# Kernel optimization log

Measured on AMD Instinct MI355X. Metric: run time of the kernel, lower is better.

The kernel has to match this reference:

```python
import jax, jax.numpy as jnp
import numpy as np

N = 49998      # num nodes, divisible by (neg_sample_ratio + 2) = 3
E = 800000     # num edges (avg degree 16)
DIM_IN = 128
DIM_OUT = 32
H0 = 8         # heads layer 0
H1 = 1         # heads layer 1


def setup_inputs() -> dict:
    key = jax.random.key(0)
    ks = jax.random.split(key, 16)
    s = 0.05
    x = jax.random.normal(ks[0], (N, DIM_IN), dtype=jnp.float32)
    src = jax.random.randint(ks[1], (E,), 0, N)
    dst = jax.random.randint(ks[2], (E,), 0, N)
    W0 = jax.random.normal(ks[3], (DIM_IN, H0 * DIM_OUT), dtype=jnp.float32) * s
    al0 = jax.random.normal(ks[4], (H0, DIM_OUT), dtype=jnp.float32) * s
    ar0 = jax.random.normal(ks[5], (H0, DIM_OUT), dtype=jnp.float32) * s
    b0 = jnp.zeros((H0 * DIM_OUT,), dtype=jnp.float32)
    W1 = jax.random.normal(ks[6], (H0 * DIM_OUT, H1 * DIM_OUT), dtype=jnp.float32) * s
    al1 = jax.random.normal(ks[7], (H1, DIM_OUT), dtype=jnp.float32) * s
    ar1 = jax.random.normal(ks[8], (H1, DIM_OUT), dtype=jnp.float32) * s
    b1 = jnp.zeros((H1 * DIM_OUT,), dtype=jnp.float32)
    P1 = jax.random.normal(ks[9], (DIM_OUT, DIM_OUT), dtype=jnp.float32) * s
    pb1 = jnp.zeros((DIM_OUT,), dtype=jnp.float32)
    P2 = jax.random.normal(ks[10], (DIM_OUT, DIM_OUT), dtype=jnp.float32) * s
    pb2 = jnp.zeros((DIM_OUT,), dtype=jnp.float32)
    P3 = jax.random.normal(ks[11], (DIM_OUT, 1), dtype=jnp.float32) * s
    pb3 = jnp.zeros((1,), dtype=jnp.float32)
    return dict(x=x, src=src, dst=dst, neg_sample_ratio=1,
                W0=W0, al0=al0, ar0=ar0, b0=b0,
                W1=W1, al1=al1, ar1=ar1, b1=b1,
                P1=P1, pb1=pb1, P2=P2, pb2=pb2, P3=P3, pb3=pb3)


def gat_conv(x, src, dst, W, al, ar, b):
    """DGL GATConv: linear proj -> edge LeakyReLU score -> per-dst segment softmax -> weighted scatter-sum + bias."""
    n = x.shape[0]
    H, D = al.shape
    f = (x @ W).reshape(n, H, D)                     # [N,H,D]
    el = jnp.sum(f * al, axis=-1)                    # [N,H]
    er = jnp.sum(f * ar, axis=-1)                    # [N,H]
    e = jax.nn.leaky_relu(el[src] + er[dst], 0.2)    # [E,H] edge scores
    m = jax.ops.segment_max(e, dst, num_segments=n)  # [N,H] stable softmax max
    a = jnp.exp(e - m[dst])                          # [E,H]
    denom = jax.ops.segment_sum(a, dst, num_segments=n)  # [N,H]
    a = a / denom[dst]                               # normalized attention
    out = jax.ops.segment_sum(a[:, :, None] * f[src], dst, num_segments=n)  # [N,H,D]
    return out + b.reshape(1, H, D)


def reference(x, src, dst, neg_sample_ratio,
              W0, al0, ar0, b0, W1, al1, ar1, b1,
              P1, pb1, P2, pb2, P3, pb3):
    # layer 0: GATConv with ELU activation, flatten heads
    h = jax.nn.elu(gat_conv(x, src, dst, W0, al0, ar0, b0)).reshape(x.shape[0], -1)
    # layer 1: GATConv, no activation, mean over heads
    h = gat_conv(h, src, dst, W1, al1, ar1, b1).mean(axis=1)  # [N, DIM_OUT]

    num_edge = h.shape[0] // (neg_sample_ratio + 2)
    src_h = h[:num_edge]
    pos_dst_h = h[num_edge:2 * num_edge]
    neg_dst_h = h[2 * num_edge:]

    def predictor(z):
        z = jax.nn.relu(z @ P1 + pb1)
        z = jax.nn.relu(z @ P2 + pb2)
        return z @ P3 + pb3

    h_pos = predictor(src_h * pos_dst_h)
    h_neg = predictor(jnp.tile(src_h, (neg_sample_ratio, 1)) * neg_dst_h)
    return (h_pos, h_neg)
```

## Files before the change

### kernel.cpp

```cpp
#include <hip/hip_runtime.h>
#include <hip/hip_fp16.h>
#include <cmath>

#define CAPB 64
#define CAPF 88
#define CAP1 96
#define WA   92
#define G0_ROWS 32
#define G0_PAD 36
#define NSCAT 1024

typedef _Float16 h2v __attribute__((ext_vector_type(2)));

__device__ __forceinline__ float dot2a(unsigned f, unsigned w, float acc) {
  return __builtin_amdgcn_fdot2(__builtin_bit_cast(h2v, f),
                                __builtin_bit_cast(h2v, w), acc, false);
}
__device__ __forceinline__ unsigned pkh2(float lo, float hi) {
  return (unsigned)__half_as_ushort(__float2half_rn(lo)) |
         ((unsigned)__half_as_ushort(__float2half_rn(hi)) << 16);
}

__global__ void k_prep(const float* __restrict__ W0, const float* __restrict__ W1,
                       unsigned* __restrict__ W0h, unsigned* __restrict__ W1ct,
                       int* __restrict__ cnt, int Np1) {
  int gid = blockIdx.x * 256 + threadIdx.x;
  int stride = gridDim.x * 256;
  for (int i = gid; i < Np1; i += stride) cnt[i] = 0;
  if (gid < 16384) {
    int k2 = gid >> 8, c = gid & 255;
    W0h[gid] = pkh2(W0[(size_t)(2 * k2) * 256 + c], W0[(size_t)(2 * k2 + 1) * 256 + c]);
  } else if (gid < 20480) {
    int j = gid - 16384;
    int c = j >> 7, k2 = j & 127;
    W1ct[j] = pkh2(W1[(size_t)(2 * k2) * 32 + c], W1[(size_t)(2 * k2 + 1) * 32 + c]);
  } else if (gid < 20992) {
    W0h[gid - 20992 + 16896] = 0;
  }
}

__global__ void k_gemm0_scatter(const float* __restrict__ x, const unsigned* __restrict__ W0h,
                                const float* __restrict__ al, const float* __restrict__ ar,
                                const int* __restrict__ dst, const int* __restrict__ src,
                                unsigned short* __restrict__ f0h, float* __restrict__ el,
                                float* __restrict__ er, int* __restrict__ cnt,
                                int* __restrict__ ovf_cnt, int* __restrict__ bpad,
                                int* __restrict__ ovf, int N, int E, int ngemm) {
  __shared__ unsigned s_x2[66 * G0_PAD];
  int t = threadIdx.x;

  if (blockIdx.x >= ngemm) {
    int nscat = gridDim.x - ngemm;
    for (int e = (blockIdx.x - ngemm) * blockDim.x + t; e < E; e += nscat * blockDim.x) {
      int d = dst[e];
      int pos = atomicAdd(&cnt[d], 1);
      if (pos < CAPB) bpad[(size_t)d * CAPB + pos] = src[e];
      else { int op = atomicAdd(ovf_cnt, 1); ovf[op] = e; }
    }
    return;
  }

  int w = t >> 6, l = t & 63;
  int row0 = blockIdx.x * G0_ROWS;
  {
    int row = t & 31, cg = t >> 5;
    int grow = row0 + row; if (grow >= N) grow = N - 1;
    const float* xp = x + (size_t)grow * 128 + cg * 16;
    int k2b = cg * 8;
#pragma unroll
    for (int j = 0; j < 4; ++j) {
      float4 v = *(const float4*)(xp + 4 * j);
      s_x2[(k2b + 2 * j) * G0_PAD + row] = pkh2(v.x, v.y);
      s_x2[(k2b + 2 * j + 1) * G0_PAD + row] = pkh2(v.z, v.w);
    }
  }
  __syncthreads();

  float4 acc[8];
#pragma unroll
  for (int r = 0; r < 8; ++r) acc[r] = make_float4(0.f, 0.f, 0.f, 0.f);

  const unsigned* wp = W0h + 4 * l;
  int rbase = w * 8;

#define LDX(dstv, kk)                                              \
  { const unsigned* xk_ = &s_x2[(kk) * G0_PAD + rbase];            \
    *(uint4*)&dstv[0]  = *(const uint4*)(xk_);                     \
    *(uint4*)&dstv[4]  = *(const uint4*)(xk_ + 4); }
#define DOTS(xv, w4)                                               \
  _Pragma("unroll")                                                \
  for (int r = 0; r < 8; ++r) {                                    \
    acc[r].x = dot2a(xv[r], w4.x, acc[r].x);                       \
    acc[r].y = dot2a(xv[r], w4.y, acc[r].y);                       \
    acc[r].z = dot2a(xv[r], w4.z, acc[r].z);                       \
    acc[r].w = dot2a(xv[r], w4.w, acc[r].w);                       \
  }

  unsigned xA[8], xB[8];
  uint4 wA = *(const uint4*)(wp);
  uint4 wB = *(const uint4*)(wp + 256);
  LDX(xA, 0);
#pragma unroll 2
  for (int k2 = 0; k2 < 64; k2 += 2) {
    uint4 wC = *(const uint4*)(wp + (size_t)(k2 + 2) * 256);
    uint4 wD = *(const uint4*)(wp + (size_t)(k2 + 3) * 256);
    LDX(xB, k2 + 1);
    DOTS(xA, wA);
    LDX(xA, k2 + 2);
    DOTS(xB, wB);
    wA = wC; wB = wD;
  }
#undef LDX
#undef DOTS

  int hh = l >> 3;
  float4 al4 = *(const float4*)(al + 4 * l);
  float4 ar4 = *(const float4*)(ar + 4 * l);
#pragma unroll
  for (int r = 0; r < 8; ++r) {
    int row = row0 + rbase + r;
    float4 f = acc[r];
    if (row < N) {
      ushort4 h4;
      h4.x = __half_as_ushort(__float2half_rn(f.x));
      h4.y = __half_as_ushort(__float2half_rn(f.y));
      h4.z = __half_as_ushort(__float2half_rn(f.z));
      h4.w = __half_as_ushort(__float2half_rn(f.w));
      *(ushort4*)(f0h + (size_t)row * 256 + 4 * l) = h4;
    }
    float pl = fmaf(f.x, al4.x, fmaf(f.y, al4.y, fmaf(f.z, al4.z, f.w * al4.w)));
    float pr = fmaf(f.x, ar4.x, fmaf(f.y, ar4.y, fmaf(f.z, ar4.z, f.w * ar4.w)));
#pragma unroll
    for (int off = 4; off >= 1; off >>= 1) {
      pl += __shfl_xor(pl, off, 64);
      pr += __shfl_xor(pr, off, 64);
    }
    if ((l & 7) == 0 && row < N) {
      el[row * 8 + hh] = pl;
      er[row * 8 + hh] = pr;
    }
  }
}

__global__ void k_fused0(const float* __restrict__ el, const float* __restrict__ er,
                         const unsigned short* __restrict__ f0h, const int* __restrict__ cnt,
                         const int* __restrict__ ovf_cnt, const int* __restrict__ bpad,
                         const int* __restrict__ ovf, const int* __restrict__ dstp,
                         const int* __restrict__ src, const float* __restrict__ b0,
                         const unsigned* __restrict__ W1ct, const float* __restrict__ al1,
                         const float* __restrict__ ar1, unsigned short* __restrict__ f1h,
                         float* __restrict__ el1, float* __restrict__ er1, int N) {
  __shared__ unsigned s_w1[32 * 132];
  __shared__ unsigned short s_wa[8][8 * WA];
  __shared__ int s_s[8][CAPF];
  __shared__ unsigned s_h2[8][128];

  const int t = threadIdx.x;
  for (int base = t * 4; base < 4096; base += 2048) {
    uint4 v = *(const uint4*)&W1ct[base];
    int c = base >> 7, k2 = base & 127;
    *(uint4*)&s_w1[c * 132 + k2] = v;
  }
  __syncthreads();

  const int w = __builtin_amdgcn_readfirstlane(t >> 6);
  const int l = t & 63;
  const int n = blockIdx.x * 8 + w;
  if (n >= N) return;

  int* sS = s_s[w];
  unsigned short* sWA = s_wa[w];

  const int sub = l & 31, half = l >> 5, hh = sub >> 2;
  float4 b0a = ((const float4*)(b0 + 8 * sub))[0];
  float4 b0b = ((const float4*)(b0 + 8 * sub))[1];
  float al1c = al1[sub], ar1c = ar1[sub];

  int cn = cnt[n];
  int degb = cn < CAPB ? cn : CAPB;
  if (l < degb) sS[l] = bpad[(size_t)n * CAPB + l];
  int deg = degb;
  int ovl = ovf_cnt[0];
  if (ovl) {
    int d = degb;
    if (l == 0) {
      for (int j = 0; j < ovl && d < 84; ++j) {
        int e = ovf[j];
        if (dstp[e] == n) sS[d++] = src[e];
      }
    }
    deg = __shfl(d, 0, 64);
  }

  int degp = (deg + 3) & ~3;
  if (l < degp - deg) sS[deg + l] = sS[0];

#define GLOAD(AA, BB, ii)                                              \
  { int2 s_ = *(const int2*)&sS[(ii) + 2 * half];                      \
    AA = ((const uint4*)(f0h + (size_t)s_.x * 256))[sub];              \
    BB = ((const uint4*)(f0h + (size_t)s_.y * 256))[sub]; }
#define GCOMP(AA, BB, ii)                                              \
  { unsigned wpk = *(const unsigned*)&sWA[hh * WA + (ii) + 2 * half];  \
    unsigned lo_, hi_;                                                 \
    lo_ = __builtin_amdgcn_perm(AA.x, BB.x, 0x01000504u);              \
    hi_ = __builtin_amdgcn_perm(AA.x, BB.x, 0x03020706u);              \
    a0 = dot2a(lo_, wpk, a0); a1 = dot2a(hi_, wpk, a1);                \
    lo_ = __builtin_amdgcn_perm(AA.y, BB.y, 0x01000504u);              \
    hi_ = __builtin_amdgcn_perm(AA.y, BB.y, 0x03020706u);              \
    a2 = dot2a(lo_, wpk, a2); a3 = dot2a(hi_, wpk, a3);                \
    lo_ = __builtin_amdgcn_perm(AA.z, BB.z, 0x01000504u);              \
    hi_ = __builtin_amdgcn_perm(AA.z, BB.z, 0x03020706u);              \
    a4 = dot2a(lo_, wpk, a4); a5 = dot2a(hi_, wpk, a5);                \
    lo_ = __builtin_amdgcn_perm(AA.w, BB.w, 0x01000504u);              \
    hi_ = __builtin_amdgcn_perm(AA.w, BB.w, 0x03020706u);              \
    a6 = dot2a(lo_, wpk, a6); a7 = dot2a(hi_, wpk, a7); }

  uint4 A, B, A2, B2;
  if (degp > 0) {
    GLOAD(A, B, 0);
    if (degp > 4) GLOAD(A2, B2, 4);
  }

  float er_h = er[n * 8 + (l & 7)];
  float psum = 0.f;
  for (int e = l >> 3; e < deg; e += 8) {
    int sidx = sS[e];
    float v = el[sidx * 8 + (l & 7)] + er_h;
    v = v >= 0.f ? v : 0.2f * v;
    float a = __expf(v);
    sWA[(l & 7) * WA + e] = __half_as_ushort(__float2half_rn(a));
    psum += a;
  }
  psum += __shfl_xor(psum, 8, 64);
  psum += __shfl_xor(psum, 16, 64);
  psum += __shfl_xor(psum, 32, 64);
  float rs = psum > 0.f ? __builtin_amdgcn_rcpf(psum) : 0.f;

  { int pe = deg + (l >> 3); if (pe < degp) sWA[(l & 7) * WA + pe] = 0; }

  float a0 = 0.f, a1 = 0.f, a2 = 0.f, a3 = 0.f, a4 = 0.f, a5 = 0.f, a6 = 0.f, a7 = 0.f;
  if (degp > 0) {
    for (int i = 0;;) {
      GCOMP(A, B, i);
      if (i + 8 < degp) GLOAD(A, B, i + 8);
      if (i + 4 >= degp) break;
      GCOMP(A2, B2, i + 4);
      if (i + 12 < degp) GLOAD(A2, B2, i + 12);
      if (i + 8 >= degp) break;
      i += 8;
    }
  }
#undef GLOAD
#undef GCOMP
  a0 += __shfl_xor(a0, 32, 64); a1 += __shfl_xor(a1, 32, 64);
  a2 += __shfl_xor(a2, 32, 64); a3 += __shfl_xor(a3, 32, 64);
  a4 += __shfl_xor(a4, 32, 64); a5 += __shfl_xor(a5, 32, 64);
  a6 += __shfl_xor(a6, 32, 64); a7 += __shfl_xor(a7, 32, 64);

  float sc = __shfl(rs, hh, 64);
  float o0 = fmaf(a0, sc, b0a.x), o1 = fmaf(a1, sc, b0a.y);
  float o2 = fmaf(a2, sc, b0a.z), o3 = fmaf(a3, sc, b0a.w);
  float o4 = fmaf(a4, sc, b0b.x), o5 = fmaf(a5, sc, b0b.y);
  float o6 = fmaf(a6, sc, b0b.z), o7 = fmaf(a7, sc, b0b.w);
  o0 = o0 > 0.f ? o0 : __expf(o0) - 1.f;  o1 = o1 > 0.f ? o1 : __expf(o1) - 1.f;
  o2 = o2 > 0.f ? o2 : __expf(o2) - 1.f;  o3 = o3 > 0.f ? o3 : __expf(o3) - 1.f;
  o4 = o4 > 0.f ? o4 : __expf(o4) - 1.f;  o5 = o5 > 0.f ? o5 : __expf(o5) - 1.f;
  o6 = o6 > 0.f ? o6 : __expf(o6) - 1.f;  o7 = o7 > 0.f ? o7 : __expf(o7) - 1.f;
  if (half == 0) {
    uint4 hp;
    hp.x = pkh2(o0, o1); hp.y = pkh2(o2, o3);
    hp.z = pkh2(o4, o5); hp.w = pkh2(o6, o7);
    *(uint4*)&s_h2[w][4 * sub] = hp;
  }
  asm volatile("s_waitcnt lgkmcnt(0)" ::: "memory");

  const unsigned* wrow = &s_w1[sub * 132 + half * 64];
  const unsigned* hrow = &s_h2[w][half * 64];
  float p = 0.f;
#pragma unroll
  for (int j = 0; j < 64; j += 4) {
    uint4 wv = *(const uint4*)&wrow[j];
    uint4 hv = *(const uint4*)&hrow[j];
    p = dot2a(hv.x, wv.x, p);
    p = dot2a(hv.y, wv.y, p);
    p = dot2a(hv.z, wv.z, p);
    p = dot2a(hv.w, wv.w, p);
  }
  p += __shfl_xor(p, 32, 64);
  float pn = __shfl_xor(p, 1, 64);
  float pl = p * al1c, pr = p * ar1c;
#pragma unroll
  for (int off = 16; off >= 1; off >>= 1) {
    pl += __shfl_xor(pl, off, 64);
    pr += __shfl_xor(pr, off, 64);
  }
  if (half == 0 && (sub & 1) == 0)
    *(unsigned*)(f1h + (size_t)n * 32 + sub) = pkh2(p, pn);
  if (l == 0) { el1[n] = pl; er1[n] = pr; }
}

__global__ void k_fused1(const float* __restrict__ el, const float* __restrict__ er,
                         const unsigned short* __restrict__ f1h, const int* __restrict__ cnt,
                         const int* __restrict__ ovf_cnt, const int* __restrict__ bpad,
                         const int* __restrict__ ovf, const int* __restrict__ dstp,
                         const int* __restrict__ src, const float* __restrict__ b1,
                         float* __restrict__ h1, int N) {
  __shared__ int s_s[8][CAP1];
  __shared__ unsigned s_wp[8][CAP1 / 2];

  const int t = threadIdx.x;
  const int g = __builtin_amdgcn_readfirstlane(t >> 6);
  const int lane = t & 63;
  int n = blockIdx.x * 8 + g;
  int nn = n < N ? n : N - 1;
  int* sS = s_s[g];
  unsigned* sWP = s_wp[g];

  int cn = cnt[nn];
  int degb = cn < CAPB ? cn : CAPB;
  if (lane < degb) sS[lane] = bpad[(size_t)nn * CAPB + lane];
  int deg = degb;
  int ovl = ovf_cnt[0];
  if (ovl) {
    int d = degb;
    if (lane == 0) {
      for (int j = 0; j < ovl && d < CAP1 - 16; ++j) {
        int e = ovf[j];
        if (dstp[e] == nn) sS[d++] = src[e];
      }
    }
    deg = __shfl(d, 0, 64);
  }
  int degp = (deg + 15) & ~15;
  if (deg + lane < degp) sS[deg + lane] = sS[0];

  const int es = lane >> 3, q = lane & 7;
  uint2 A, B;
  if (degp > 0) {
    A = *(const uint2*)(f1h + (size_t)sS[es] * 32 + 4 * q);
    B = *(const uint2*)(f1h + (size_t)sS[es + 8] * 32 + 4 * q);
  }

  float er_n = er[nn];
  float psum = 0.f;
  for (int i0 = 0; i0 < degp; i0 += 64) {
    int i = i0 + lane;
    float a = 0.f;
    if (i < deg) {
      float v = el[sS[i]] + er_n;
      v = v >= 0.f ? v : 0.2f * v;
      a = __expf(v);
      psum += a;
    }
    float an = __shfl_xor(a, 8, 64);
    if ((lane & 15) < 8 && i < degp)
      sWP[(i0 >> 1) + ((lane >> 4) << 3) + (lane & 7)] = pkh2(a, an);
  }
#pragma unroll
  for (int off = 32; off >= 1; off >>= 1) psum += __shfl_xor(psum, off, 64);
  float rs = psum > 0.f ? __builtin_amdgcn_rcpf(psum) : 0.f;

  float c0 = 0.f, c1 = 0.f, c2 = 0.f, c3 = 0.f;
  if (degp > 0) {
    for (int i0 = 0;;) {
      int in = i0 + 16;
      uint2 A2, B2;
      if (in < degp) {
        A2 = *(const uint2*)(f1h + (size_t)sS[in + es] * 32 + 4 * q);
        B2 = *(const uint2*)(f1h + (size_t)sS[in + es + 8] * 32 + 4 * q);
      }
      unsigned wp = sWP[(i0 >> 1) + es];
      unsigned lo = __builtin_amdgcn_perm(A.x, B.x, 0x01000504u);
      unsigned hi = __builtin_amdgcn_perm(A.x, B.x, 0x03020706u);
      c0 = dot2a(lo, wp, c0); c1 = dot2a(hi, wp, c1);
      lo = __builtin_amdgcn_perm(A.y, B.y, 0x01000504u);
      hi = __builtin_amdgcn_perm(A.y, B.y, 0x03020706u);
      c2 = dot2a(lo, wp, c2); c3 = dot2a(hi, wp, c3);
      if (in >= degp) break;
      i0 = in; A = A2; B = B2;
    }
  }
#pragma unroll
  for (int off = 8; off <= 32; off <<= 1) {
    c0 += __shfl_xor(c0, off, 64); c1 += __shfl_xor(c1, off, 64);
    c2 += __shfl_xor(c2, off, 64); c3 += __shfl_xor(c3, off, 64);
  }
  if (es == 0 && n < N) {
    float4 b = *(const float4*)(b1 + 4 * q);
    float4 o;
    o.x = fmaf(c0, rs, b.x); o.y = fmaf(c1, rs, b.y);
    o.z = fmaf(c2, rs, b.z); o.w = fmaf(c3, rs, b.w);
    ((float4*)(h1 + (size_t)n * 32))[q] = o;
  }
}

__global__ void k_pred(const float* __restrict__ h1, const float* __restrict__ P1,
                       const float* __restrict__ pb1, const float* __restrict__ P2,
                       const float* __restrict__ pb2, const float* __restrict__ P3,
                       const float* __restrict__ pb3, float* __restrict__ out,
                       int num_edge, int total) {
  int t = threadIdx.x;
  int lane = t & 31, grp = t >> 5;
  int k = blockIdx.x * 8 + grp;
  int kk = k < total ? k : 0;
  float z;
  if (kk < num_edge) {
    z = h1[(size_t)kk * 32 + lane] * h1[(size_t)(kk + num_edge) * 32 + lane];
  } else {
    int i = kk - num_edge;
    int im = i;
    while (im >= num_edge) im -= num_edge;
    z = h1[(size_t)im * 32 + lane] * h1[(size_t)(2 * num_edge + i) * 32 + lane];
  }
  double a1 = 0;
#pragma unroll
  for (int d = 0; d < 32; ++d)
    a1 += (double)__shfl(z, d, 32) * (double)P1[d * 32 + lane];
  float t1 = (float)(a1 + (double)pb1[lane]);
  t1 = t1 > 0.f ? t1 : 0.f;
  double a2 = 0;
#pragma unroll
  for (int d = 0; d < 32; ++d)
    a2 += (double)__shfl(t1, d, 32) * (double)P2[d * 32 + lane];
  float t2 = (float)(a2 + (double)pb2[lane]);
  t2 = t2 > 0.f ? t2 : 0.f;
  double a3 = (double)t2 * (double)P3[lane];
#pragma unroll
  for (int off = 16; off >= 1; off >>= 1) a3 += __shfl_xor(a3, off, 64);
  if (lane == 0 && k < total) out[k] = (float)(a3 + (double)pb3[0]);
}

extern "C" void kernel_launch(void* const* d_in, const int* in_sizes, int n_in,
                              void* d_out, int out_size, void* d_ws, size_t ws_size,
                              hipStream_t stream) {
  const float* x   = (const float*)d_in[0];
  const int*   src = (const int*)d_in[1];
  const int*   dst = (const int*)d_in[2];
  const float* W0  = (const float*)d_in[4];
  const float* al0 = (const float*)d_in[5];
  const float* ar0 = (const float*)d_in[6];
  const float* b0  = (const float*)d_in[7];
  const float* W1  = (const float*)d_in[8];
  const float* al1 = (const float*)d_in[9];
  const float* ar1 = (const float*)d_in[10];
  const float* b1  = (const float*)d_in[11];
  const float* P1  = (const float*)d_in[12];
  const float* pb1 = (const float*)d_in[13];
  const float* P2  = (const float*)d_in[14];
  const float* pb2 = (const float*)d_in[15];
  const float* P3  = (const float*)d_in[16];
  const float* pb3 = (const float*)d_in[17];

  int N = in_sizes[0] / 128;
  int E = in_sizes[1];
  int num_edge = N - out_size;

  size_t off = 0;
  auto alloc = [&](size_t bytes) -> void* {
    void* p = (char*)d_ws + off;
    off += (bytes + 255) & ~(size_t)255;
    return p;
  };
  unsigned short* f0h = (unsigned short*)alloc((size_t)N * 256 * 2);
  unsigned short* f1h = (unsigned short*)alloc((size_t)N * 32 * 2);
  float* h1   = (float*)alloc((size_t)N * 32 * 4);
  float* el   = (float*)alloc((size_t)N * 8 * 4);
  float* er   = (float*)alloc((size_t)N * 8 * 4);
  float* el1  = (float*)alloc((size_t)N * 4);
  float* er1  = (float*)alloc((size_t)N * 4);
  int*   cnt  = (int*)alloc((size_t)(N + 1) * 4);
  int*   bpad = (int*)alloc((size_t)N * CAPB * 4);
  int*   ovf  = (int*)alloc((size_t)E * 4);
  unsigned* W1ct = (unsigned*)alloc(4096 * 4);
  unsigned* W0h  = (unsigned*)alloc(16896 * 4);
  if (off > ws_size) return;
  int* ovf_cnt = cnt + N;

  int ngemm = (N + G0_ROWS - 1) / G0_ROWS;
  k_prep<<<128, 256, 0, stream>>>(W0, W1, W0h, W1ct, cnt, N + 1);
  k_gemm0_scatter<<<ngemm + NSCAT, 256, 0, stream>>>(x, W0h, al0, ar0, dst, src,
                                            f0h, el, er, cnt, ovf_cnt, bpad, ovf,
                                            N, E, ngemm);
  k_fused0<<<(N + 7) / 8, 512, 0, stream>>>(el, er, f0h, cnt, ovf_cnt, bpad, ovf, dst,
                                            src, b0, W1ct, al1, ar1, f1h, el1, er1, N);
  k_fused1<<<(N + 7) / 8, 512, 0, stream>>>(el1, er1, f1h, cnt, ovf_cnt, bpad, ovf, dst,
                                            src, b1, h1, N);
  k_pred<<<(out_size + 7) / 8, 256, 0, stream>>>(h1, P1, pb1, P2, pb2, P3, pb3,
                                                 (float*)d_out, num_edge, out_size);
}
```

Before: 262.6 us.

## Split layer-1 projection out of fused aggregation kernel and shrink GEMM0 tile

```diff
diff --git a/kernel.cpp b/kernel.cpp
--- a/kernel.cpp
+++ b/kernel.cpp
@@ -6,7 +6,7 @@
 #define CAPF 88
 #define CAP1 96
 #define WA   92
-#define G0_ROWS 32
+#define G0_ROWS 16
 #define G0_PAD 36
 #define NSCAT 1024
 
@@ -63,12 +63,12 @@
   int w = t >> 6, l = t & 63;
   int row0 = blockIdx.x * G0_ROWS;
   {
-    int row = t & 31, cg = t >> 5;
+    int row = t & 15, cg = t >> 4;
     int grow = row0 + row; if (grow >= N) grow = N - 1;
-    const float* xp = x + (size_t)grow * 128 + cg * 16;
-    int k2b = cg * 8;
-#pragma unroll
-    for (int j = 0; j < 4; ++j) {
+    const float* xp = x + (size_t)grow * 128 + cg * 8;
+    int k2b = cg * 4;
+#pragma unroll
+    for (int j = 0; j < 2; ++j) {
       float4 v = *(const float4*)(xp + 4 * j);
       s_x2[(k2b + 2 * j) * G0_PAD + row] = pkh2(v.x, v.y);
       s_x2[(k2b + 2 * j + 1) * G0_PAD + row] = pkh2(v.z, v.w);
@@ -76,27 +76,25 @@
   }
   __syncthreads();
 
-  float4 acc[8];
-#pragma unroll
-  for (int r = 0; r < 8; ++r) acc[r] = make_float4(0.f, 0.f, 0.f, 0.f);
+  float4 acc[4];
+#pragma unroll
+  for (int r = 0; r < 4; ++r) acc[r] = make_float4(0.f, 0.f, 0.f, 0.f);
 
   const unsigned* wp = W0h + 4 * l;
-  int rbase = w * 8;
+  int rbase = w * 4;
 
 #define LDX(dstv, kk)                                              \
-  { const unsigned* xk_ = &s_x2[(kk) * G0_PAD + rbase];            \
-    *(uint4*)&dstv[0]  = *(const uint4*)(xk_);                     \
-    *(uint4*)&dstv[4]  = *(const uint4*)(xk_ + 4); }
+  { *(uint4*)&dstv[0] = *(const uint4*)&s_x2[(kk) * G0_PAD + rbase]; }
 #define DOTS(xv, w4)                                               \
   _Pragma("unroll")                                                \
-  for (int r = 0; r < 8; ++r) {                                    \
+  for (int r = 0; r < 4; ++r) {                                    \
     acc[r].x = dot2a(xv[r], w4.x, acc[r].x);                       \
     acc[r].y = dot2a(xv[r], w4.y, acc[r].y);                       \
     acc[r].z = dot2a(xv[r], w4.z, acc[r].z);                       \
     acc[r].w = dot2a(xv[r], w4.w, acc[r].w);                       \
   }
 
-  unsigned xA[8], xB[8];
+  unsigned xA[4], xB[4];
   uint4 wA = *(const uint4*)(wp);
   uint4 wB = *(const uint4*)(wp + 256);
   LDX(xA, 0);
@@ -117,7 +115,7 @@
   float4 al4 = *(const float4*)(al + 4 * l);
   float4 ar4 = *(const float4*)(ar + 4 * l);
 #pragma unroll
-  for (int r = 0; r < 8; ++r) {
+  for (int r = 0; r < 4; ++r) {
     int row = row0 + rbase + r;
     float4 f = acc[r];
     if (row < N) {
@@ -147,25 +145,14 @@
                          const int* __restrict__ ovf_cnt, const int* __restrict__ bpad,
                          const int* __restrict__ ovf, const int* __restrict__ dstp,
                          const int* __restrict__ src, const float* __restrict__ b0,
-                         const unsigned* __restrict__ W1ct, const float* __restrict__ al1,
-                         const float* __restrict__ ar1, unsigned short* __restrict__ f1h,
-                         float* __restrict__ el1, float* __restrict__ er1, int N) {
-  __shared__ unsigned s_w1[32 * 132];
-  __shared__ unsigned short s_wa[8][8 * WA];
-  __shared__ int s_s[8][CAPF];
-  __shared__ unsigned s_h2[8][128];
+                         unsigned* __restrict__ h2g, int N) {
+  __shared__ unsigned short s_wa[4][8 * WA];
+  __shared__ int s_s[4][CAPF];
 
   const int t = threadIdx.x;
-  for (int base = t * 4; base < 4096; base += 2048) {
-    uint4 v = *(const uint4*)&W1ct[base];
-    int c = base >> 7, k2 = base & 127;
-    *(uint4*)&s_w1[c * 132 + k2] = v;
-  }
-  __syncthreads();
-
   const int w = __builtin_amdgcn_readfirstlane(t >> 6);
   const int l = t & 63;
-  const int n = blockIdx.x * 8 + w;
+  const int n = blockIdx.x * 4 + w;
   if (n >= N) return;
 
   int* sS = s_s[w];
@@ -174,7 +161,6 @@
   const int sub = l & 31, half = l >> 5, hh = sub >> 2;
   float4 b0a = ((const float4*)(b0 + 8 * sub))[0];
   float4 b0b = ((const float4*)(b0 + 8 * sub))[1];
-  float al1c = al1[sub], ar1c = ar1[sub];
 
   int cn = cnt[n];
   int degb = cn < CAPB ? cn : CAPB;
@@ -270,33 +256,57 @@
     uint4 hp;
     hp.x = pkh2(o0, o1); hp.y = pkh2(o2, o3);
     hp.z = pkh2(o4, o5); hp.w = pkh2(o6, o7);
-    *(uint4*)&s_h2[w][4 * sub] = hp;
-  }
-  asm volatile("s_waitcnt lgkmcnt(0)" ::: "memory");
-
-  const unsigned* wrow = &s_w1[sub * 132 + half * 64];
-  const unsigned* hrow = &s_h2[w][half * 64];
+    *(uint4*)(h2g + (size_t)n * 128 + 4 * sub) = hp;
+  }
+}
+
+__global__ void k_gemm1(const unsigned* __restrict__ h2g, const unsigned* __restrict__ W1ct,
+                        const float* __restrict__ al1, const float* __restrict__ ar1,
+                        unsigned short* __restrict__ f1h, float* __restrict__ el1,
+                        float* __restrict__ er1, int N) {
+  __shared__ unsigned s_w1[32 * 132];
+  __shared__ unsigned s_h[8 * 128];
+
+  const int t = threadIdx.x;
+  const int n0 = blockIdx.x * 8;
+  for (int base = t * 4; base < 4096; base += 1024) {
+    uint4 v = *(const uint4*)&W1ct[base];
+    int c = base >> 7, k2 = base & 127;
+    *(uint4*)&s_w1[c * 132 + k2] = v;
+  }
+  {
+    int r = t >> 5, wi = t & 31;
+    int row = n0 + r; if (row >= N) row = N - 1;
+    uint4 v = *(const uint4*)(h2g + (size_t)row * 128 + wi * 4);
+    *(uint4*)&s_h[r * 128 + wi * 4] = v;
+  }
+  __syncthreads();
+
+  const int r = t >> 5, c = t & 31;
+  const int n = n0 + r;
+  const unsigned* hrow = &s_h[r * 128];
+  const unsigned* wrow = &s_w1[c * 132];
   float p = 0.f;
-#pragma unroll
-  for (int j = 0; j < 64; j += 4) {
+#pragma unroll 8
+  for (int j = 0; j < 128; j += 4) {
+    uint4 hv = *(const uint4*)&hrow[j];
     uint4 wv = *(const uint4*)&wrow[j];
-    uint4 hv = *(const uint4*)&hrow[j];
     p = dot2a(hv.x, wv.x, p);
     p = dot2a(hv.y, wv.y, p);
     p = dot2a(hv.z, wv.z, p);
     p = dot2a(hv.w, wv.w, p);
   }
-  p += __shfl_xor(p, 32, 64);
-  float pn = __shfl_xor(p, 1, 64);
-  float pl = p * al1c, pr = p * ar1c;
+  float pl = p * al1[c], pr = p * ar1[c];
 #pragma unroll
   for (int off = 16; off >= 1; off >>= 1) {
-    pl += __shfl_xor(pl, off, 64);
-    pr += __shfl_xor(pr, off, 64);
-  }
-  if (half == 0 && (sub & 1) == 0)
-    *(unsigned*)(f1h + (size_t)n * 32 + sub) = pkh2(p, pn);
-  if (l == 0) { el1[n] = pl; er1[n] = pr; }
+    pl += __shfl_xor(pl, off, 32);
+    pr += __shfl_xor(pr, off, 32);
+  }
+  float pn = __shfl_xor(p, 1, 32);
+  if (n < N) {
+    if ((c & 1) == 0) *(unsigned*)(f1h + (size_t)n * 32 + c) = pkh2(p, pn);
+    if (c == 0) { el1[n] = pl; er1[n] = pr; }
+  }
 }
 
 __global__ void k_fused1(const float* __restrict__ el, const float* __restrict__ er,
@@ -462,6 +472,7 @@
     return p;
   };
   unsigned short* f0h = (unsigned short*)alloc((size_t)N * 256 * 2);
+  unsigned* h2g = (unsigned*)alloc((size_t)N * 128 * 4);
   unsigned short* f1h = (unsigned short*)alloc((size_t)N * 32 * 2);
   float* h1   = (float*)alloc((size_t)N * 32 * 4);
   float* el   = (float*)alloc((size_t)N * 8 * 4);
@@ -481,8 +492,9 @@
   k_gemm0_scatter<<<ngemm + NSCAT, 256, 0, stream>>>(x, W0h, al0, ar0, dst, src,
                                             f0h, el, er, cnt, ovf_cnt, bpad, ovf,
                                             N, E, ngemm);
-  k_fused0<<<(N + 7) / 8, 512, 0, stream>>>(el, er, f0h, cnt, ovf_cnt, bpad, ovf, dst,
-                                            src, b0, W1ct, al1, ar1, f1h, el1, er1, N);
+  k_fused0<<<(N + 3) / 4, 256, 0, stream>>>(el, er, f0h, cnt, ovf_cnt, bpad, ovf, dst,
+                                            src, b0, h2g, N);
+  k_gemm1<<<(N + 7) / 8, 256, 0, stream>>>(h2g, W1ct, al1, ar1, f1h, el1, er1, N);
   k_fused1<<<(N + 7) / 8, 512, 0, stream>>>(el1, er1, f1h, cnt, ovf_cnt, bpad, ovf, dst,
                                             src, b1, h1, N);
   k_pred<<<(out_size + 7) / 8, 256, 0, stream>>>(h1, P1, pb1, P2, pb2, P3, pb3,
```

After: 295.2 us. +12.4%, slower.

## Stage W0 chunks through double-buffered LDS in layer-0 GEMM

Applied to the files above, without the earlier changes.

```diff
diff --git a/kernel.cpp b/kernel.cpp
--- a/kernel.cpp
+++ b/kernel.cpp
@@ -34,8 +34,6 @@
     int j = gid - 16384;
     int c = j >> 7, k2 = j & 127;
     W1ct[j] = pkh2(W1[(size_t)(2 * k2) * 32 + c], W1[(size_t)(2 * k2 + 1) * 32 + c]);
-  } else if (gid < 20992) {
-    W0h[gid - 20992 + 16896] = 0;
   }
 }
 
@@ -46,7 +44,8 @@
                                 float* __restrict__ er, int* __restrict__ cnt,
                                 int* __restrict__ ovf_cnt, int* __restrict__ bpad,
                                 int* __restrict__ ovf, int N, int E, int ngemm) {
-  __shared__ unsigned s_x2[66 * G0_PAD];
+  __shared__ unsigned s_x2[64 * G0_PAD];
+  __shared__ unsigned s_w0[2][8 * 256];
   int t = threadIdx.x;
 
   if (blockIdx.x >= ngemm) {
@@ -74,44 +73,42 @@
       s_x2[(k2b + 2 * j + 1) * G0_PAD + row] = pkh2(v.z, v.w);
     }
   }
-  __syncthreads();
 
   float4 acc[8];
 #pragma unroll
   for (int r = 0; r < 8; ++r) acc[r] = make_float4(0.f, 0.f, 0.f, 0.f);
 
-  const unsigned* wp = W0h + 4 * l;
   int rbase = w * 8;
 
-#define LDX(dstv, kk)                                              \
-  { const unsigned* xk_ = &s_x2[(kk) * G0_PAD + rbase];            \
-    *(uint4*)&dstv[0]  = *(const uint4*)(xk_);                     \
-    *(uint4*)&dstv[4]  = *(const uint4*)(xk_ + 4); }
-#define DOTS(xv, w4)                                               \
-  _Pragma("unroll")                                                \
-  for (int r = 0; r < 8; ++r) {                                    \
-    acc[r].x = dot2a(xv[r], w4.x, acc[r].x);                       \
-    acc[r].y = dot2a(xv[r], w4.y, acc[r].y);                       \
-    acc[r].z = dot2a(xv[r], w4.z, acc[r].z);                       \
-    acc[r].w = dot2a(xv[r], w4.w, acc[r].w);                       \
-  }
-
-  unsigned xA[8], xB[8];
-  uint4 wA = *(const uint4*)(wp);
-  uint4 wB = *(const uint4*)(wp + 256);
-  LDX(xA, 0);
-#pragma unroll 2
-  for (int k2 = 0; k2 < 64; k2 += 2) {
-    uint4 wC = *(const uint4*)(wp + (size_t)(k2 + 2) * 256);
-    uint4 wD = *(const uint4*)(wp + (size_t)(k2 + 3) * 256);
-    LDX(xB, k2 + 1);
-    DOTS(xA, wA);
-    LDX(xA, k2 + 2);
-    DOTS(xB, wB);
-    wA = wC; wB = wD;
-  }
-#undef LDX
-#undef DOTS
+  uint4 rA = *(const uint4*)(W0h + t * 4);
+  uint4 rB = *(const uint4*)(W0h + 1024 + t * 4);
+
+  for (int c = 0; c < 8; ++c) {
+    *(uint4*)&s_w0[c & 1][t * 4] = rA;
+    *(uint4*)&s_w0[c & 1][1024 + t * 4] = rB;
+    if (c + 1 < 8) {
+      rA = *(const uint4*)(W0h + (c + 1) * 2048 + t * 4);
+      rB = *(const uint4*)(W0h + (c + 1) * 2048 + 1024 + t * 4);
+    }
+    __syncthreads();
+    const unsigned* wb = s_w0[c & 1];
+#pragma unroll
+    for (int k2r = 0; k2r < 8; ++k2r) {
+      int k2 = c * 8 + k2r;
+      uint4 w4 = *(const uint4*)&wb[k2r * 256 + 4 * l];
+      unsigned xv[8];
+      const unsigned* xk_ = &s_x2[k2 * G0_PAD + rbase];
+      *(uint4*)&xv[0] = *(const uint4*)(xk_);
+      *(uint4*)&xv[4] = *(const uint4*)(xk_ + 4);
+#pragma unroll
+      for (int r = 0; r < 8; ++r) {
+        acc[r].x = dot2a(xv[r], w4.x, acc[r].x);
+        acc[r].y = dot2a(xv[r], w4.y, acc[r].y);
+        acc[r].z = dot2a(xv[r], w4.z, acc[r].z);
+        acc[r].w = dot2a(xv[r], w4.w, acc[r].w);
+      }
+    }
+  }
 
   int hh = l >> 3;
   float4 al4 = *(const float4*)(al + 4 * l);
@@ -472,7 +469,7 @@
   int*   bpad = (int*)alloc((size_t)N * CAPB * 4);
   int*   ovf  = (int*)alloc((size_t)E * 4);
   unsigned* W1ct = (unsigned*)alloc(4096 * 4);
-  unsigned* W0h  = (unsigned*)alloc(16896 * 4);
+  unsigned* W0h  = (unsigned*)alloc(16384 * 4);
   if (off > ws_size) return;
   int* ovf_cnt = cnt + N;
 
```

New measurement: 289.9 us. 10.4% more time.

## Use persistent grid-stride waves in fused GAT kernels with prefetch of next node's adjacency

Applied to the files above, without the earlier changes.

```diff
diff --git a/kernel.cpp b/kernel.cpp
--- a/kernel.cpp
+++ b/kernel.cpp
@@ -9,6 +9,7 @@
 #define G0_ROWS 32
 #define G0_PAD 36
 #define NSCAT 1024
+#define PBLK 1024
 
 typedef _Float16 h2v __attribute__((ext_vector_type(2)));
 
@@ -165,8 +166,9 @@
 
   const int w = __builtin_amdgcn_readfirstlane(t >> 6);
   const int l = t & 63;
-  const int n = blockIdx.x * 8 + w;
-  if (n >= N) return;
+  const int stride = gridDim.x * 8;
+  int node = blockIdx.x * 8 + w;
+  if (node >= N) return;
 
   int* sS = s_s[w];
   unsigned short* sWA = s_wa[w];
@@ -175,25 +177,10 @@
   float4 b0a = ((const float4*)(b0 + 8 * sub))[0];
   float4 b0b = ((const float4*)(b0 + 8 * sub))[1];
   float al1c = al1[sub], ar1c = ar1[sub];
-
-  int cn = cnt[n];
-  int degb = cn < CAPB ? cn : CAPB;
-  if (l < degb) sS[l] = bpad[(size_t)n * CAPB + l];
-  int deg = degb;
-  int ovl = ovf_cnt[0];
-  if (ovl) {
-    int d = degb;
-    if (l == 0) {
-      for (int j = 0; j < ovl && d < 84; ++j) {
-        int e = ovf[j];
-        if (dstp[e] == n) sS[d++] = src[e];
-      }
-    }
-    deg = __shfl(d, 0, 64);
-  }
-
-  int degp = (deg + 3) & ~3;
-  if (l < degp - deg) sS[deg + l] = sS[0];
+  const int ovl = ovf_cnt[0];
+
+  int cur_cn = cnt[node];
+  int cur_bp = bpad[(size_t)node * CAPB + l];
 
 #define GLOAD(AA, BB, ii)                                              \
   { int2 s_ = *(const int2*)&sS[(ii) + 2 * half];                      \
@@ -215,88 +202,119 @@
     hi_ = __builtin_amdgcn_perm(AA.w, BB.w, 0x03020706u);              \
     a6 = dot2a(lo_, wpk, a6); a7 = dot2a(hi_, wpk, a7); }
 
-  uint4 A, B, A2, B2;
-  if (degp > 0) {
-    GLOAD(A, B, 0);
-    if (degp > 4) GLOAD(A2, B2, 4);
-  }
-
-  float er_h = er[n * 8 + (l & 7)];
-  float psum = 0.f;
-  for (int e = l >> 3; e < deg; e += 8) {
-    int sidx = sS[e];
-    float v = el[sidx * 8 + (l & 7)] + er_h;
-    v = v >= 0.f ? v : 0.2f * v;
-    float a = __expf(v);
-    sWA[(l & 7) * WA + e] = __half_as_ushort(__float2half_rn(a));
-    psum += a;
-  }
-  psum += __shfl_xor(psum, 8, 64);
-  psum += __shfl_xor(psum, 16, 64);
-  psum += __shfl_xor(psum, 32, 64);
-  float rs = psum > 0.f ? __builtin_amdgcn_rcpf(psum) : 0.f;
-
-  { int pe = deg + (l >> 3); if (pe < degp) sWA[(l & 7) * WA + pe] = 0; }
-
-  float a0 = 0.f, a1 = 0.f, a2 = 0.f, a3 = 0.f, a4 = 0.f, a5 = 0.f, a6 = 0.f, a7 = 0.f;
-  if (degp > 0) {
-    for (int i = 0;;) {
-      GCOMP(A, B, i);
-      if (i + 8 < degp) GLOAD(A, B, i + 8);
-      if (i + 4 >= degp) break;
-      GCOMP(A2, B2, i + 4);
-      if (i + 12 < degp) GLOAD(A2, B2, i + 12);
-      if (i + 8 >= degp) break;
-      i += 8;
-    }
+  while (true) {
+    const int n = node;
+    int cn = cur_cn;
+    int bpv = cur_bp;
+    const int nxt = node + stride;
+    if (nxt < N) {
+      cur_cn = cnt[nxt];
+      cur_bp = bpad[(size_t)nxt * CAPB + l];
+    }
+
+    int degb = cn < CAPB ? cn : CAPB;
+    if (l < degb) sS[l] = bpv;
+    int deg = degb;
+    if (ovl) {
+      int d = degb;
+      if (l == 0) {
+        for (int j = 0; j < ovl && d < 84; ++j) {
+          int e = ovf[j];
+          if (dstp[e] == n) sS[d++] = src[e];
+        }
+      }
+      deg = __shfl(d, 0, 64);
+    }
+
+    int degp = (deg + 3) & ~3;
+    if (l < degp - deg) sS[deg + l] = sS[0];
+
+    uint4 A, B, A2, B2;
+    if (degp > 0) {
+      GLOAD(A, B, 0);
+      if (degp > 4) GLOAD(A2, B2, 4);
+    }
+
+    float er_h = er[n * 8 + (l & 7)];
+    float psum = 0.f;
+    for (int e = l >> 3; e < deg; e += 8) {
+      int sidx = sS[e];
+      float v = el[sidx * 8 + (l & 7)] + er_h;
+      v = v >= 0.f ? v : 0.2f * v;
+      float a = __expf(v);
+      sWA[(l & 7) * WA + e] = __half_as_ushort(__float2half_rn(a));
+      psum += a;
+    }
+    psum += __shfl_xor(psum, 8, 64);
+    psum += __shfl_xor(psum, 16, 64);
+    psum += __shfl_xor(psum, 32, 64);
+    float rs = psum > 0.f ? __builtin_amdgcn_rcpf(psum) : 0.f;
+
+    { int pe = deg + (l >> 3); if (pe < degp) sWA[(l & 7) * WA + pe] = 0; }
+
+    float a0 = 0.f, a1 = 0.f, a2 = 0.f, a3 = 0.f, a4 = 0.f, a5 = 0.f, a6 = 0.f, a7 = 0.f;
+    if (degp > 0) {
+      for (int i = 0;;) {
+        GCOMP(A, B, i);
+        if (i + 8 < degp) GLOAD(A, B, i + 8);
+        if (i + 4 >= degp) break;
+        GCOMP(A2, B2, i + 4);
+        if (i + 12 < degp) GLOAD(A2, B2, i + 12);
+        if (i + 8 >= degp) break;
+        i += 8;
+      }
+    }
+    a0 += __shfl_xor(a0, 32, 64); a1 += __shfl_xor(a1, 32, 64);
+    a2 += __shfl_xor(a2, 32, 64); a3 += __shfl_xor(a3, 32, 64);
+    a4 += __shfl_xor(a4, 32, 64); a5 += __shfl_xor(a5, 32, 64);
+    a6 += __shfl_xor(a6, 32, 64); a7 += __shfl_xor(a7, 32, 64);
+
+    float sc = __shfl(rs, hh, 64);
+    float o0 = fmaf(a0, sc, b0a.x), o1 = fmaf(a1, sc, b0a.y);
+    float o2 = fmaf(a2, sc, b0a.z), o3 = fmaf(a3, sc, b0a.w);
+    float o4 = fmaf(a4, sc, b0b.x), o5 = fmaf(a5, sc, b0b.y);
+    float o6 = fmaf(a6, sc, b0b.z), o7 = fmaf(a7, sc, b0b.w);
+    o0 = o0 > 0.f ? o0 : __expf(o0) - 1.f;  o1 = o1 > 0.f ? o1 : __expf(o1) - 1.f;
+    o2 = o2 > 0.f ? o2 : __expf(o2) - 1.f;  o3 = o3 > 0.f ? o3 : __expf(o3) - 1.f;
+    o4 = o4 > 0.f ? o4 : __expf(o4) - 1.f;  o5 = o5 > 0.f ? o5 : __expf(o5) - 1.f;
+    o6 = o6 > 0.f ? o6 : __expf(o6) - 1.f;  o7 = o7 > 0.f ? o7 : __expf(o7) - 1.f;
+    if (half == 0) {
+      uint4 hp;
+      hp.x = pkh2(o0, o1); hp.y = pkh2(o2, o3);
+      hp.z = pkh2(o4, o5); hp.w = pkh2(o6, o7);
+      *(uint4*)&s_h2[w][4 * sub] = hp;
+    }
+    asm volatile("s_waitcnt lgkmcnt(0)" ::: "memory");
+
+    const unsigned* wrow = &s_w1[sub * 132 + half * 64];
+    const unsigned* hrow = &s_h2[w][half * 64];
+    float p = 0.f;
+#pragma unroll
+    for (int j = 0; j < 64; j += 4) {
+      uint4 wv = *(const uint4*)&wrow[j];
+      uint4 hv = *(const uint4*)&hrow[j];
+      p = dot2a(hv.x, wv.x, p);
+      p = dot2a(hv.y, wv.y, p);
+      p = dot2a(hv.z, wv.z, p);
+      p = dot2a(hv.w, wv.w, p);
+    }
+    p += __shfl_xor(p, 32, 64);
+    float pn = __shfl_xor(p, 1, 64);
+    float pl = p * al1c, pr = p * ar1c;
+#pragma unroll
+    for (int off = 16; off >= 1; off >>= 1) {
+      pl += __shfl_xor(pl, off, 64);
+      pr += __shfl_xor(pr, off, 64);
+    }
+    if (half == 0 && (sub & 1) == 0)
+      *(unsigned*)(f1h + (size_t)n * 32 + sub) = pkh2(p, pn);
+    if (l == 0) { el1[n] = pl; er1[n] = pr; }
+
+    if (nxt >= N) break;
+    node = nxt;
   }
 #undef GLOAD
 #undef GCOMP
-  a0 += __shfl_xor(a0, 32, 64); a1 += __shfl_xor(a1, 32, 64);
-  a2 += __shfl_xor(a2, 32, 64); a3 += __shfl_xor(a3, 32, 64);
-  a4 += __shfl_xor(a4, 32, 64); a5 += __shfl_xor(a5, 32, 64);
-  a6 += __shfl_xor(a6, 32, 64); a7 += __shfl_xor(a7, 32, 64);
-
-  float sc = __shfl(rs, hh, 64);
-  float o0 = fmaf(a0, sc, b0a.x), o1 = fmaf(a1, sc, b0a.y);
-  float o2 = fmaf(a2, sc, b0a.z), o3 = fmaf(a3, sc, b0a.w);
-  float o4 = fmaf(a4, sc, b0b.x), o5 = fmaf(a5, sc, b0b.y);
-  float o6 = fmaf(a6, sc, b0b.z), o7 = fmaf(a7, sc, b0b.w);
-  o0 = o0 > 0.f ? o0 : __expf(o0) - 1.f;  o1 = o1 > 0.f ? o1 : __expf(o1) - 1.f;
-  o2 = o2 > 0.f ? o2 : __expf(o2) - 1.f;  o3 = o3 > 0.f ? o3 : __expf(o3) - 1.f;
-  o4 = o4 > 0.f ? o4 : __expf(o4) - 1.f;  o5 = o5 > 0.f ? o5 : __expf(o5) - 1.f;
-  o6 = o6 > 0.f ? o6 : __expf(o6) - 1.f;  o7 = o7 > 0.f ? o7 : __expf(o7) - 1.f;
-  if (half == 0) {
-    uint4 hp;
-    hp.x = pkh2(o0, o1); hp.y = pkh2(o2, o3);
-    hp.z = pkh2(o4, o5); hp.w = pkh2(o6, o7);
-    *(uint4*)&s_h2[w][4 * sub] = hp;
-  }
-  asm volatile("s_waitcnt lgkmcnt(0)" ::: "memory");
-
-  const unsigned* wrow = &s_w1[sub * 132 + half * 64];
-  const unsigned* hrow = &s_h2[w][half * 64];
-  float p = 0.f;
-#pragma unroll
-  for (int j = 0; j < 64; j += 4) {
-    uint4 wv = *(const uint4*)&wrow[j];
-    uint4 hv = *(const uint4*)&hrow[j];
-    p = dot2a(hv.x, wv.x, p);
-    p = dot2a(hv.y, wv.y, p);
-    p = dot2a(hv.z, wv.z, p);
-    p = dot2a(hv.w, wv.w, p);
-  }
-  p += __shfl_xor(p, 32, 64);
-  float pn = __shfl_xor(p, 1, 64);
-  float pl = p * al1c, pr = p * ar1c;
-#pragma unroll
-  for (int off = 16; off >= 1; off >>= 1) {
-    pl += __shfl_xor(pl, off, 64);
-    pr += __shfl_xor(pr, off, 64);
-  }
-  if (half == 0 && (sub & 1) == 0)
-    *(unsigned*)(f1h + (size_t)n * 32 + sub) = pkh2(p, pn);
-  if (l == 0) { el1[n] = pl; er1[n] = pr; }
 }
 
 __global__ void k_fused1(const float* __restrict__ el, const float* __restrict__ er,
@@ -311,86 +329,104 @@
   const int t = threadIdx.x;
   const int g = __builtin_amdgcn_readfirstlane(t >> 6);
   const int lane = t & 63;
-  int n = blockIdx.x * 8 + g;
-  int nn = n < N ? n : N - 1;
+  const int stride = gridDim.x * 8;
+  int node = blockIdx.x * 8 + g;
+  if (node >= N) return;
   int* sS = s_s[g];
   unsigned* sWP = s_wp[g];
 
-  int cn = cnt[nn];
-  int degb = cn < CAPB ? cn : CAPB;
-  if (lane < degb) sS[lane] = bpad[(size_t)nn * CAPB + lane];
-  int deg = degb;
-  int ovl = ovf_cnt[0];
-  if (ovl) {
-    int d = degb;
-    if (lane == 0) {
-      for (int j = 0; j < ovl && d < CAP1 - 16; ++j) {
-        int e = ovf[j];
-        if (dstp[e] == nn) sS[d++] = src[e];
+  const int es = lane >> 3, q = lane & 7;
+  const int ovl = ovf_cnt[0];
+  float4 bb = *(const float4*)(b1 + 4 * q);
+
+  int cur_cn = cnt[node];
+  int cur_bp = bpad[(size_t)node * CAPB + lane];
+
+  while (true) {
+    const int n = node;
+    int cn = cur_cn;
+    int bpv = cur_bp;
+    const int nxt = node + stride;
+    if (nxt < N) {
+      cur_cn = cnt[nxt];
+      cur_bp = bpad[(size_t)nxt * CAPB + lane];
+    }
+
+    int degb = cn < CAPB ? cn : CAPB;
+    if (lane < degb) sS[lane] = bpv;
+    int deg = degb;
+    if (ovl) {
+      int d = degb;
+      if (lane == 0) {
+        for (int j = 0; j < ovl && d < CAP1 - 16; ++j) {
+          int e = ovf[j];
+          if (dstp[e] == n) sS[d++] = src[e];
+        }
       }
-    }
-    deg = __shfl(d, 0, 64);
-  }
-  int degp = (deg + 15) & ~15;
-  if (deg + lane < degp) sS[deg + lane] = sS[0];
-
-  const int es = lane >> 3, q = lane & 7;
-  uint2 A, B;
-  if (degp > 0) {
-    A = *(const uint2*)(f1h + (size_t)sS[es] * 32 + 4 * q);
-    B = *(const uint2*)(f1h + (size_t)sS[es + 8] * 32 + 4 * q);
-  }
-
-  float er_n = er[nn];
-  float psum = 0.f;
-  for (int i0 = 0; i0 < degp; i0 += 64) {
-    int i = i0 + lane;
-    float a = 0.f;
-    if (i < deg) {
-      float v = el[sS[i]] + er_n;
-      v = v >= 0.f ? v : 0.2f * v;
-      a = __expf(v);
-      psum += a;
-    }
-    float an = __shfl_xor(a, 8, 64);
-    if ((lane & 15) < 8 && i < degp)
-      sWP[(i0 >> 1) + ((lane >> 4) << 3) + (lane & 7)] = pkh2(a, an);
-  }
-#pragma unroll
-  for (int off = 32; off >= 1; off >>= 1) psum += __shfl_xor(psum, off, 64);
-  float rs = psum > 0.f ? __builtin_amdgcn_rcpf(psum) : 0.f;
-
-  float c0 = 0.f, c1 = 0.f, c2 = 0.f, c3 = 0.f;
-  if (degp > 0) {
-    for (int i0 = 0;;) {
-      int in = i0 + 16;
-      uint2 A2, B2;
-      if (in < degp) {
-        A2 = *(const uint2*)(f1h + (size_t)sS[in + es] * 32 + 4 * q);
-        B2 = *(const uint2*)(f1h + (size_t)sS[in + es + 8] * 32 + 4 * q);
+      deg = __shfl(d, 0, 64);
+    }
+    int degp = (deg + 15) & ~15;
+    if (deg + lane < degp) sS[deg + lane] = sS[0];
+
+    uint2 A, B;
+    if (degp > 0) {
+      A = *(const uint2*)(f1h + (size_t)sS[es] * 32 + 4 * q);
+      B = *(const uint2*)(f1h + (size_t)sS[es + 8] * 32 + 4 * q);
+    }
+
+    float er_n = er[n];
+    float psum = 0.f;
+    for (int i0 = 0; i0 < degp; i0 += 64) {
+      int i = i0 + lane;
+      float a = 0.f;
+      if (i < deg) {
+        float v = el[sS[i]] + er_n;
+        v = v >= 0.f ? v : 0.2f * v;
+        a = __expf(v);
+        psum += a;
       }
-      unsigned wp = sWP[(i0 >> 1) + es];
-      unsigned lo = __builtin_amdgcn_perm(A.x, B.x, 0x01000504u);
-      unsigned hi = __builtin_amdgcn_perm(A.x, B.x, 0x03020706u);
-      c0 = dot2a(lo, wp, c0); c1 = dot2a(hi, wp, c1);
-      lo = __builtin_amdgcn_perm(A.y, B.y, 0x01000504u);
-      hi = __builtin_amdgcn_perm(A.y, B.y, 0x03020706u);
-      c2 = dot2a(lo, wp, c2); c3 = dot2a(hi, wp, c3);
-      if (in >= degp) break;
-      i0 = in; A = A2; B = B2;
-    }
-  }
-#pragma unroll
-  for (int off = 8; off <= 32; off <<= 1) {
-    c0 += __shfl_xor(c0, off, 64); c1 += __shfl_xor(c1, off, 64);
-    c2 += __shfl_xor(c2, off, 64); c3 += __shfl_xor(c3, off, 64);
-  }
-  if (es == 0 && n < N) {
-    float4 b = *(const float4*)(b1 + 4 * q);
-    float4 o;
-    o.x = fmaf(c0, rs, b.x); o.y = fmaf(c1, rs, b.y);
-    o.z = fmaf(c2, rs, b.z); o.w = fmaf(c3, rs, b.w);
-    ((float4*)(h1 + (size_t)n * 32))[q] = o;
+      float an = __shfl_xor(a, 8, 64);
+      if ((lane & 15) < 8 && i < degp)
+        sWP[(i0 >> 1) + ((lane >> 4) << 3) + (lane & 7)] = pkh2(a, an);
+    }
+#pragma unroll
+    for (int off = 32; off >= 1; off >>= 1) psum += __shfl_xor(psum, off, 64);
+    float rs = psum > 0.f ? __builtin_amdgcn_rcpf(psum) : 0.f;
+
+    float c0 = 0.f, c1 = 0.f, c2 = 0.f, c3 = 0.f;
+    if (degp > 0) {
+      for (int i0 = 0;;) {
+        int in = i0 + 16;
+        uint2 A2, B2;
+        if (in < degp) {
+          A2 = *(const uint2*)(f1h + (size_t)sS[in + es] * 32 + 4 * q);
+          B2 = *(const uint2*)(f1h + (size_t)sS[in + es + 8] * 32 + 4 * q);
+        }
+        unsigned wp = sWP[(i0 >> 1) + es];
+        unsigned lo = __builtin_amdgcn_perm(A.x, B.x, 0x01000504u);
+        unsigned hi = __builtin_amdgcn_perm(A.x, B.x, 0x03020706u);
+        c0 = dot2a(lo, wp, c0); c1 = dot2a(hi, wp, c1);
+        lo = __builtin_amdgcn_perm(A.y, B.y, 0x01000504u);
+        hi = __builtin_amdgcn_perm(A.y, B.y, 0x03020706u);
+        c2 = dot2a(lo, wp, c2); c3 = dot2a(hi, wp, c3);
+        if (in >= degp) break;
+        i0 = in; A = A2; B = B2;
+      }
+    }
+#pragma unroll
+    for (int off = 8; off <= 32; off <<= 1) {
+      c0 += __shfl_xor(c0, off, 64); c1 += __shfl_xor(c1, off, 64);
+      c2 += __shfl_xor(c2, off, 64); c3 += __shfl_xor(c3, off, 64);
+    }
+    if (es == 0) {
+      float4 o;
+      o.x = fmaf(c0, rs, bb.x); o.y = fmaf(c1, rs, bb.y);
+      o.z = fmaf(c2, rs, bb.z); o.w = fmaf(c3, rs, bb.w);
+      ((float4*)(h1 + (size_t)n * 32))[q] = o;
+    }
+
+    if (nxt >= N) break;
+    node = nxt;
   }
 }
 
@@ -481,10 +517,10 @@
   k_gemm0_scatter<<<ngemm + NSCAT, 256, 0, stream>>>(x, W0h, al0, ar0, dst, src,
                                             f0h, el, er, cnt, ovf_cnt, bpad, ovf,
                                             N, E, ngemm);
-  k_fused0<<<(N + 7) / 8, 512, 0, stream>>>(el, er, f0h, cnt, ovf_cnt, bpad, ovf, dst,
-                                            src, b0, W1ct, al1, ar1, f1h, el1, er1, N);
-  k_fused1<<<(N + 7) / 8, 512, 0, stream>>>(el1, er1, f1h, cnt, ovf_cnt, bpad, ovf, dst,
-                                            src, b1, h1, N);
+  k_fused0<<<PBLK, 512, 0, stream>>>(el, er, f0h, cnt, ovf_cnt, bpad, ovf, dst,
+                                     src, b0, W1ct, al1, ar1, f1h, el1, er1, N);
+  k_fused1<<<PBLK, 512, 0, stream>>>(el1, er1, f1h, cnt, ovf_cnt, bpad, ovf, dst,
+                                     src, b1, h1, N);
   k_pred<<<(out_size + 7) / 8, 256, 0, stream>>>(h1, P1, pb1, P2, pb2, P3, pb3,
                                                  (float*)d_out, num_edge, out_size);
 }
```

Result: no change. 266.5 us (+1.5%).
